# Kernel optimization log

Hardware: AMD Instinct MI355X
Metric: run time of the kernel (lower is better)

Reference implementation:

```python
import jax, jax.numpy as jnp
import numpy as np

DEPTH, DIM, M_DIM, K = 3, 16, 16, 8  # depth, emb_dim, EGNN m_dim default, num_nearest_neighbors
LN_EPS = 1e-5


def _gather(x, idx):
    # x: [B,L,...], idx: [B,L,K] -> [B,L,K,...] (per-batch neighbor gather)
    return jax.vmap(lambda xb, ib: xb[ib])(x, idx)


def _lin(k, fi, fo):
    k1, k2 = jax.random.split(k)
    lim = 1.0 / np.sqrt(fi)
    w = jax.random.uniform(k1, (fi, fo), minval=-lim, maxval=lim, dtype=jnp.float32)
    b = jax.random.uniform(k2, (fo,), minval=-lim, maxval=lim, dtype=jnp.float32)
    return w, b


def _stacked(k, fi, fo):
    ws, bs = zip(*[_lin(kk, fi, fo) for kk in jax.random.split(k, DEPTH)])
    return jnp.stack(ws), jnp.stack(bs)


def setup_inputs() -> dict:
    key = jax.random.key(0)
    ks = jax.random.split(key, 16)
    B, L, num_tokens = 16, 1024, 2
    edge_in = 2 * DIM + 1  # feats_i, feats_j, rel_dist
    inp = {}
    inp['coords'] = jax.random.normal(ks[0], (B, L, 3), dtype=jnp.float32) * 3.0
    inp['residues'] = jax.random.randint(ks[1], (B, L), 0, num_tokens)
    inp['lengths'] = jax.random.randint(ks[2], (B,), L // 2, L + 1)
    inp['token_emb'] = jax.random.normal(ks[3], (num_tokens, DIM), dtype=jnp.float32)
    inp['pos_emb'] = jax.random.normal(ks[4], (L, DIM), dtype=jnp.float32)
    inp['edge_w1'], inp['edge_b1'] = _stacked(ks[5], edge_in, edge_in * 2)
    inp['edge_w2'], inp['edge_b2'] = _stacked(ks[6], edge_in * 2, M_DIM)
    inp['coors_w1'], inp['coors_b1'] = _stacked(ks[7], M_DIM, M_DIM * 4)
    inp['coors_w2'], inp['coors_b2'] = _stacked(ks[8], M_DIM * 4, 1)
    inp['ln_g'] = jnp.ones((DEPTH, DIM), jnp.float32)
    inp['ln_b'] = jnp.zeros((DEPTH, DIM), jnp.float32)
    inp['node_w1'], inp['node_b1'] = _stacked(ks[9], DIM + M_DIM, DIM * 2)
    inp['node_w2'], inp['node_b2'] = _stacked(ks[10], DIM * 2, DIM)
    inp['final_w'], inp['final_b'] = _lin(ks[11], DIM, 3)
    return inp


def reference(coords, residues, lengths, token_emb, pos_emb,
              edge_w1, edge_b1, edge_w2, edge_b2,
              coors_w1, coors_b1, coors_w2, coors_b2,
              ln_g, ln_b, node_w1, node_b1, node_w2, node_b2,
              final_w, final_b):
    B, L, _ = coords.shape
    silu = jax.nn.silu
    mask = jnp.arange(L)[None, :] < lengths[:, None]                 # [B,L]
    pair_mask = mask[:, :, None] & mask[:, None, :]                  # [B,L,L]
    eye = jnp.eye(L, dtype=bool)
    # chain adjacency: i <-> i+1 where both endpoints are within length
    r = jnp.arange(L - 1)
    chain = jnp.zeros((L, L), bool).at[r, r + 1].set(True)
    chain = chain | chain.T
    adj = (chain[None] & pair_mask) & ~eye                           # [B,L,L]

    feats = token_emb[residues] + pos_emb[None, :L]                  # [B,L,D]
    coors = coords
    for d in range(DEPTH):
        # pairwise squared distances for kNN ranking (memory-bound)
        rel_dist_full = jnp.sum((coors[:, :, None] - coors[:, None, :]) ** 2, -1)  # [B,L,L]
        ranking = jnp.where(pair_mask, rel_dist_full, 1e5)
        ranking = jnp.where(eye, -1.0, ranking)   # self always selected first
        ranking = jnp.where(adj, 0.0, ranking)    # adjacency edges forced in
        _, idx = jax.lax.top_k(-ranking, K)                           # [B,L,K] smallest
        mask_j = _gather(mask, idx)
        emask = mask[:, :, None] & mask_j                             # [B,L,K] (valid_radius=inf)
        coors_j = _gather(coors, idx)                                 # [B,L,K,3]
        rel_coors = coors[:, :, None] - coors_j                       # [B,L,K,3]
        rel_dist = jnp.sum(rel_coors ** 2, -1, keepdims=True)         # [B,L,K,1]
        feats_j = _gather(feats, idx)                                 # [B,L,K,D]
        feats_i = jnp.broadcast_to(feats[:, :, None], feats_j.shape)
        edge_in = jnp.concatenate([feats_i, feats_j, rel_dist], -1)   # [B,L,K,2D+1]
        h = silu(edge_in @ edge_w1[d] + edge_b1[d])
        m_ij = silu(h @ edge_w2[d] + edge_b2[d])                      # [B,L,K,M]
        # equivariant coordinate update
        w = silu(m_ij @ coors_w1[d] + coors_b1[d]) @ coors_w2[d] + coors_b2[d]
        w = jnp.where(emask[..., None], w, 0.0)[..., 0]               # [B,L,K]
        coors = coors + jnp.einsum('blk,blkc->blc', w, rel_coors)
        # node update (norm_feats=True in EGNN_Network -> LayerNorm)
        m_i = jnp.sum(jnp.where(emask[..., None], m_ij, 0.0), 2)      # [B,L,M]
        mu = feats.mean(-1, keepdims=True)
        var = jnp.mean((feats - mu) ** 2, -1, keepdims=True)
        normed = (feats - mu) / jnp.sqrt(var + LN_EPS) * ln_g[d] + ln_b[d]
        nin = jnp.concatenate([normed, m_i], -1)                      # [B,L,D+M]
        feats = feats + (silu(nin @ node_w1[d] + node_b1[d]) @ node_w2[d] + node_b2[d])
    delta = feats @ final_w + final_b                                 # [B,L,3]
    return delta
```

## Files before the change

kernel.cpp:

```cpp
#include <hip/hip_runtime.h>
#include <math.h>

typedef unsigned long long u64;
typedef unsigned int u32;

#define NB 16
#define SL 1024
#define DIM 16
#define MDIM 16
#define KNN 8
#define CH 64
#define NHID 32
#define LN_EPS 1e-5f
#define PST 144

__device__ __forceinline__ float silu_f(float x) {
    const float e = __expf(-x);
    return x * __builtin_amdgcn_rcpf(1.0f + e);
}

__global__ __launch_bounds__(256) void init_kernel(
    const float* __restrict__ coords, const int* __restrict__ residues,
    const float* __restrict__ token_emb, const float* __restrict__ pos_emb,
    const float* __restrict__ w1tp, const float* __restrict__ g_eb1,
    float* __restrict__ coordsA, float* __restrict__ featsA,
    float* __restrict__ Pout)
{
    const int t = blockIdx.x * 256 + threadIdx.x;
    const int node = t >> 2;
    const int part = t & 3;
    const int l = node & (SL - 1);
    const int r = residues[node];
    float f[16];
    {
        const float4* te = (const float4*)(token_emb + (size_t)r * DIM);
        const float4* pe = (const float4*)(pos_emb + (size_t)l * DIM);
#pragma unroll
        for (int q = 0; q < 4; ++q) {
            float4 a = te[q], b4 = pe[q];
            f[4*q+0] = a.x + b4.x; f[4*q+1] = a.y + b4.y;
            f[4*q+2] = a.z + b4.z; f[4*q+3] = a.w + b4.w;
        }
    }
    if (part == 0) {
        float4* fo = (float4*)(featsA + (size_t)node * DIM);
#pragma unroll
        for (int q = 0; q < 4; ++q)
            fo[q] = make_float4(f[4*q], f[4*q+1], f[4*q+2], f[4*q+3]);
        coordsA[node * 3 + 0] = coords[node * 3 + 0];
        coordsA[node * 3 + 1] = coords[node * 3 + 1];
        coordsA[node * 3 + 2] = coords[node * 3 + 2];
    }
    const int ubase = (part & 1) * 33;
    const int wbase = (part < 2) ? 0 : 66;
    float res[36];
    res[33] = 0.f; res[34] = 0.f; res[35] = 0.f;
#pragma unroll
    for (int oo = 0; oo < 33; ++oo) {
        const int u = ubase + oo;
        const float* wr = w1tp + (wbase + u) * 16;
        float a0 = (part < 2) ? g_eb1[u] : 0.0f;
        float a1 = 0.f, a2 = 0.f, a3 = 0.f;
#pragma unroll
        for (int c = 0; c < 16; c += 4) {
            a0 = fmaf(f[c + 0], wr[c + 0], a0);
            a1 = fmaf(f[c + 1], wr[c + 1], a1);
            a2 = fmaf(f[c + 2], wr[c + 2], a2);
            a3 = fmaf(f[c + 3], wr[c + 3], a3);
        }
        res[oo] = (a0 + a1) + (a2 + a3);
    }
    float4* op = (float4*)(Pout + (size_t)node * PST + part * 36);
#pragma unroll
    for (int q = 0; q < 9; ++q)
        op[q] = make_float4(res[4*q], res[4*q+1], res[4*q+2], res[4*q+3]);
}

__global__ __launch_bounds__(256) void pack_kernel(
    const float* __restrict__ ew1, const float* __restrict__ ew2,
    const float* __restrict__ cw1,
    const float* __restrict__ nw1, const float* __restrict__ nw2,
    float* __restrict__ w1tp, float* __restrict__ w1rp, float* __restrict__ w2p,
    float* __restrict__ cw1t, float* __restrict__ nw1t, float* __restrict__ nw2t)
{
    const int stride = gridDim.x * 256;
    const int t0 = blockIdx.x * 256 + threadIdx.x;
    for (int idx = t0; idx < 3 * 132 * 16; idx += stride) {
        int d = idx / (132 * 16); int r = idx - d * 132 * 16; int o = r >> 4; int c = r & 15;
        int u = (o < 66) ? o : (o - 66);
        int cc = (o < 66) ? c : (16 + c);
        w1tp[idx] = ew1[(d * 33 + cc) * 66 + u];
    }
    for (int idx = t0; idx < 3 * 72; idx += stride) {
        int d = idx / 72; int o = idx - d * 72; int hh = o / 36; int uu = o - hh * 36;
        w1rp[idx] = (uu < 33) ? ew1[(d * 33 + 32) * 66 + hh * 33 + uu] : 0.0f;
    }
    for (int idx = t0; idx < 3 * 72 * 16; idx += stride) {
        int d = idx / (72 * 16); int r = idx - d * 72 * 16; int u = r >> 4; int v = r & 15;
        int hh = u / 36; int uu = u - hh * 36;
        w2p[idx] = (uu < 33) ? ew2[(d * 66 + hh * 33 + uu) * 16 + v] : 0.0f;
    }
    for (int idx = t0; idx < 3 * CH * 16; idx += stride) {
        int d = idx / (CH * 16); int r = idx - d * CH * 16; int t = r >> 4; int v = r & 15;
        cw1t[(d * CH + t) * 16 + v] = cw1[(d * 16 + v) * CH + t];
    }
    for (int idx = t0; idx < 3 * NHID * 32; idx += stride) {
        int d = idx / (NHID * 32); int r = idx - d * NHID * 32; int u = r >> 5; int c = r & 31;
        nw1t[(d * NHID + u) * 32 + c] = nw1[(d * 32 + c) * NHID + u];
    }
    for (int idx = t0; idx < 3 * 16 * 32; idx += stride) {
        int d = idx / (16 * 32); int r = idx - d * 16 * 32; int c = r >> 5; int u = r & 31;
        nw2t[(d * 16 + c) * 32 + u] = nw2[(d * 32 + u) * 16 + c];
    }
}

__device__ __forceinline__ void merge8(u32* a, const u32* bb) {
    u32 c[8];
#pragma unroll
    for (int t = 0; t < 8; ++t) c[t] = min(a[t], bb[7 - t]);
#define MCAS(x, y) { u32 mn = min(c[x], c[y]); u32 mx = max(c[x], c[y]); c[x] = mn; c[y] = mx; }
    MCAS(0, 4) MCAS(1, 5) MCAS(2, 6) MCAS(3, 7)
    MCAS(0, 2) MCAS(1, 3) MCAS(4, 6) MCAS(5, 7)
    MCAS(0, 1) MCAS(2, 3) MCAS(4, 5) MCAS(6, 7)
#undef MCAS
#pragma unroll
    for (int t = 0; t < 8; ++t) a[t] = c[t];
}

__global__ __launch_bounds__(1024) void knn_kernel(
    const float* __restrict__ coords, const int* __restrict__ lengths,
    int* __restrict__ idxbuf)
{
    __shared__ __align__(16) float4 s_cand[SL];
    __shared__ u32 lists[16][64][9];
    const int tid = threadIdx.x;
    const int b = blockIdx.x >> 4;
    const int i0 = (blockIdx.x & 15) << 6;
    const int len = lengths[b];
    const float* cb = coords + (size_t)b * SL * 3;
    for (int idx = tid; idx < SL; idx += 1024) {
        const float* cp = cb + idx * 3;
        s_cand[idx] = make_float4(cp[0], cp[1], cp[2], 0.0f);
    }
    __syncthreads();

    const int wv = tid >> 6;
    const int lane = tid & 63;
    const int i = i0 + lane;
    const bool mi = i < len;
    const float4 qi = s_cand[i];
    const float xi = qi.x, yi = qi.y, zi = qi.z;

    u32 lst[8];
#pragma unroll
    for (int t = 0; t < 8; ++t) lst[t] = 0xFFFFFFFFu;

    const int jbase = wv << 6;
#pragma unroll 4
    for (int jj = 0; jj < 64; ++jj) {
        const int j = jbase + jj;
        const float4 cj = s_cand[j];
        const float dx = xi - cj.x, dy = yi - cj.y, dz = zi - cj.z;
        const float dist = dx * dx + dy * dy + dz * dz;
        const int dij = j - i;
        const bool pm = mi && (j < len);
        const bool adjx = (dij == 1) | (dij == -1);
        float v = pm ? (adjx ? 0.0f : dist) : 1e5f;
        v = (dij == 0) ? -1.0f : v;
        u32 bits = __float_as_uint(v);
        bits ^= (u32)((int)bits >> 31) | 0x80000000u;
        const u32 key = (bits & 0xFFFFFC00u) | (u32)j;
#pragma unroll
        for (int p = 7; p >= 1; --p)
            lst[p] = min(max(key, lst[p - 1]), lst[p]);
        lst[0] = min(key, lst[0]);
    }

#pragma unroll
    for (int t = 0; t < 8; ++t) lists[wv][lane][t] = lst[t];
    __syncthreads();

    if (tid < 512) {
        const int p = tid >> 6, q = tid & 63;
        u32 a[8], bb[8];
#pragma unroll
        for (int t = 0; t < 8; ++t) { a[t] = lists[2 * p][q][t]; bb[t] = lists[2 * p + 1][q][t]; }
        merge8(a, bb);
#pragma unroll
        for (int t = 0; t < 8; ++t) lists[2 * p][q][t] = a[t];
    }
    __syncthreads();
    if (tid < 256) {
        const int p = tid >> 6, q = tid & 63;
        u32 a[8], bb[8];
#pragma unroll
        for (int t = 0; t < 8; ++t) { a[t] = lists[4 * p][q][t]; bb[t] = lists[4 * p + 2][q][t]; }
        merge8(a, bb);
#pragma unroll
        for (int t = 0; t < 8; ++t) lists[4 * p][q][t] = a[t];
    }
    __syncthreads();
    if (tid < 128) {
        const int p = tid >> 6, q = tid & 63;
        u32 a[8], bb[8];
#pragma unroll
        for (int t = 0; t < 8; ++t) { a[t] = lists[8 * p][q][t]; bb[t] = lists[8 * p + 4][q][t]; }
        merge8(a, bb);
#pragma unroll
        for (int t = 0; t < 8; ++t) lists[8 * p][q][t] = a[t];
    }
    __syncthreads();
    if (tid < 64) {
        const int q = tid;
        u32 a[8], bb[8];
#pragma unroll
        for (int t = 0; t < 8; ++t) { a[t] = lists[0][q][t]; bb[t] = lists[8][q][t]; }
        merge8(a, bb);
        const size_t node = (size_t)b * SL + i0 + q;
        int4 r0 = make_int4((int)(a[0] & 1023u), (int)(a[1] & 1023u), (int)(a[2] & 1023u), (int)(a[3] & 1023u));
        int4 r1 = make_int4((int)(a[4] & 1023u), (int)(a[5] & 1023u), (int)(a[6] & 1023u), (int)(a[7] & 1023u));
        ((int4*)idxbuf)[node * 2 + 0] = r0;
        ((int4*)idxbuf)[node * 2 + 1] = r1;
    }
}

__global__ __launch_bounds__(256, 4) void layer_kernel(
    const int d,
    const float* __restrict__ coordsIn, float* __restrict__ coordsOut,
    const float* __restrict__ featsIn, float* __restrict__ featsOut,
    const float* __restrict__ Pbuf,
    const int* __restrict__ idxbuf, const int* __restrict__ lengths,
    const float* __restrict__ w1rp, const float* __restrict__ w2p,
    const float* __restrict__ g_eb2,
    const float* __restrict__ cw1t, const float* __restrict__ g_cb1,
    const float* __restrict__ g_cw2, const float* __restrict__ g_cb2,
    const float* __restrict__ g_lng, const float* __restrict__ g_lnb,
    const float* __restrict__ nw1t, const float* __restrict__ g_nb1,
    const float* __restrict__ nw2t, const float* __restrict__ g_nb2,
    const float* __restrict__ w1tp_all, const float* __restrict__ g_eb1,
    float* __restrict__ PbufOut)
{
    __shared__ float s_w2e[72 * 16];
    __shared__ float s_w1r[72];
    __shared__ float s_cw1[CH * 16];
    __shared__ float s_cw2v[CH];
    __shared__ float s_nw1[NHID * 36];
    __shared__ float s_nw2[16 * 36];
    __shared__ float s_eb2[16], s_cb1[CH];
    __shared__ float s_lng[16], s_lnb[16], s_nb1[32], s_nb2[16];
    __shared__ float s_cb2v;

    const int tid = threadIdx.x;
    for (int t = tid; t < 72 * 16; t += 256) s_w2e[t] = w2p[d * 72 * 16 + t];
    for (int t = tid; t < CH * 16; t += 256) s_cw1[t] = cw1t[d * CH * 16 + t];
    for (int t = tid; t < NHID * 32; t += 256) s_nw1[(t >> 5) * 36 + (t & 31)] = nw1t[d * NHID * 32 + t];
    for (int t = tid; t < 16 * 32; t += 256) s_nw2[(t >> 5) * 36 + (t & 31)] = nw2t[d * 16 * 32 + t];
    if (tid < 72) s_w1r[tid] = w1rp[d * 72 + tid];
    if (tid < CH) { s_cw2v[tid] = g_cw2[d * CH + tid]; s_cb1[tid] = g_cb1[d * CH + tid]; }
    if (tid < 16) {
        s_eb2[tid] = g_eb2[d * 16 + tid];
        s_lng[tid] = g_lng[d * 16 + tid];
        s_lnb[tid] = g_lnb[d * 16 + tid];
        s_nb2[tid] = g_nb2[d * 16 + tid];
    }
    if (tid < 32) s_nb1[tid] = g_nb1[d * 32 + tid];
    if (tid == 0) s_cb2v = g_cb2[d];

    const int lane = tid & 63;
    const int h = (lane >> 3) & 1;
    const int k = lane & 7;
    const int n = blockIdx.x * 16 + (tid >> 4);
    const int b = n >> 10;
    const int i = n & (SL - 1);
    const int len = lengths[b];
    const int j = idxbuf[n * 8 + k];
    const bool em = (i < len) && (j < len);

    float fi[16];
    {
        const float4* pp = (const float4*)(featsIn + (size_t)n * DIM);
        float4 a = pp[0], c2 = pp[1], c3 = pp[2], c4 = pp[3];
        fi[0]=a.x; fi[1]=a.y; fi[2]=a.z; fi[3]=a.w;
        fi[4]=c2.x; fi[5]=c2.y; fi[6]=c2.z; fi[7]=c2.w;
        fi[8]=c3.x; fi[9]=c3.y; fi[10]=c3.z; fi[11]=c3.w;
        fi[12]=c4.x; fi[13]=c4.y; fi[14]=c4.z; fi[15]=c4.w;
    }
    float ci[3], rel[3];
    {
        const float* cp = coordsIn + (size_t)n * 3;
        const float* cq = coordsIn + ((size_t)b * SL + j) * 3;
        ci[0] = cp[0]; ci[1] = cp[1]; ci[2] = cp[2];
        rel[0] = ci[0] - cq[0]; rel[1] = ci[1] - cq[1]; rel[2] = ci[2] - cq[2];
    }
    const float rd = fmaf(rel[0], rel[0], fmaf(rel[1], rel[1], rel[2] * rel[2]));

    const int ub = h * 36;
    const float* PiP = Pbuf + (size_t)n * PST + ub;
    const float* PjP = Pbuf + ((size_t)b * SL + j) * PST + 72 + ub;
    float4 pa = *(const float4*)PiP;
    float4 pb = *(const float4*)PjP;

    __syncthreads();

    float macc[16];
#pragma unroll
    for (int v = 0; v < 16; ++v) macc[v] = h ? 0.0f : s_eb2[v];
#pragma unroll
    for (int c4 = 0; c4 < 9; ++c4) {
        float4 na, nb;
        if (c4 < 8) {
            na = *(const float4*)(PiP + 4 * (c4 + 1));
            nb = *(const float4*)(PjP + 4 * (c4 + 1));
        }
        const int u0 = ub + c4 * 4;
        const float hu0 = silu_f(fmaf(rd, s_w1r[u0 + 0], pa.x + pb.x));
        const float hu1 = silu_f(fmaf(rd, s_w1r[u0 + 1], pa.y + pb.y));
        const float hu2 = silu_f(fmaf(rd, s_w1r[u0 + 2], pa.z + pb.z));
        const float hu3 = silu_f(fmaf(rd, s_w1r[u0 + 3], pa.w + pb.w));
        const float* w2r = &s_w2e[u0 * 16];
#pragma unroll
        for (int v = 0; v < 16; ++v) {
            float m0 = fmaf(hu0, w2r[v], macc[v]);
            float m1 = fmaf(hu1, w2r[16 + v], m0);
            float m2 = fmaf(hu2, w2r[32 + v], m1);
            macc[v] = fmaf(hu3, w2r[48 + v], m2);
        }
        if (c4 < 8) { pa = na; pb = nb; }
    }

    float mm[16];
#pragma unroll
    for (int v = 0; v < 16; ++v)
        mm[v] = silu_f(macc[v] + __shfl_xor(macc[v], 8, 64));

    const int tb = h * 32;
    float wa = 0.f;
#pragma unroll 4
    for (int tt = 0; tt < 32; ++tt) {
        const float* cr = &s_cw1[(tb + tt) * 16];
        float a0 = s_cb1[tb + tt], a1 = 0.f;
#pragma unroll
        for (int v = 0; v < 16; v += 2) {
            a0 = fmaf(mm[v], cr[v], a0);
            a1 = fmaf(mm[v + 1], cr[v + 1], a1);
        }
        wa = fmaf(silu_f(a0 + a1), s_cw2v[tb + tt], wa);
    }
    const float wao = __shfl_xor(wa, 8, 64);
    const float we = em ? (wa + wao + s_cb2v) : 0.f;

    float wr0 = we * rel[0], wr1 = we * rel[1], wr2 = we * rel[2];
#pragma unroll
    for (int s = 1; s < 8; s <<= 1) {
        wr0 += __shfl_xor(wr0, s, 64);
        wr1 += __shfl_xor(wr1, s, 64);
        wr2 += __shfl_xor(wr2, s, 64);
    }
    if ((lane & 15) == 0) {
        coordsOut[(size_t)n * 3 + 0] = ci[0] + wr0;
        coordsOut[(size_t)n * 3 + 1] = ci[1] + wr1;
        coordsOut[(size_t)n * 3 + 2] = ci[2] + wr2;
    }

    float mi_[16];
#pragma unroll
    for (int v = 0; v < 16; ++v) mi_[v] = em ? mm[v] : 0.f;
#pragma unroll
    for (int s = 1; s < 8; s <<= 1) {
#pragma unroll
        for (int v = 0; v < 16; ++v) mi_[v] += __shfl_xor(mi_[v], s, 64);
    }

    float mu = 0.f;
#pragma unroll
    for (int c = 0; c < 16; ++c) mu += fi[c];
    mu *= 0.0625f;
    float var = 0.f;
#pragma unroll
    for (int c = 0; c < 16; ++c) { const float dd = fi[c] - mu; var = fmaf(dd, dd, var); }
    var *= 0.0625f;
    const float rs = rsqrtf(var + LN_EPS);
    float nn[16];
#pragma unroll
    for (int c = 0; c < 16; ++c) nn[c] = fmaf((fi[c] - mu) * rs, s_lng[c], s_lnb[c]);

    const int sub = lane & 15;
    float nh[2];
#pragma unroll
    for (int q = 0; q < 2; ++q) {
        const int u = sub * 2 + q;
        const float* nr = &s_nw1[u * 36];
        float a0 = s_nb1[u], a1 = 0.f;
#pragma unroll
        for (int c = 0; c < 16; c += 2) {
            a0 = fmaf(nn[c], nr[c], a0);
            a1 = fmaf(nn[c + 1], nr[c + 1], a1);
        }
#pragma unroll
        for (int v = 0; v < 16; v += 2) {
            a0 = fmaf(mi_[v], nr[16 + v], a0);
            a1 = fmaf(mi_[v + 1], nr[16 + v + 1], a1);
        }
        nh[q] = silu_f(a0 + a1);
    }

    const int nbase = lane & ~15;
    const float* w2c = &s_nw2[sub * 36];
    float o0 = s_nb2[sub];
#pragma unroll
    for (int u = 0; u < 32; ++u) {
        const float v = __shfl(nh[u & 1], nbase + (u >> 1), 64);
        o0 = fmaf(v, w2c[u], o0);
    }
    const float fo = fi[sub] + o0;
    featsOut[(size_t)n * DIM + sub] = fo;

    if (d < 2) {
        float fr[16];
#pragma unroll
        for (int c = 0; c < 16; ++c) fr[c] = __shfl(fo, nbase + c, 64);
        const float* wbase = w1tp_all + (d + 1) * 132 * 16;
        const float* bbase = g_eb1 + (d + 1) * 66;
        float* Pout = PbufOut + (size_t)n * PST;
#pragma unroll
        for (int q = 0; q < 9; ++q) {
            const int col = sub + (q << 4);
            const int ch = (col >= 108) ? 3 : (col >= 72) ? 2 : (col >= 36) ? 1 : 0;
            const int uu = col - ch * 36;
            const bool valid = uu < 33;
            const int u = ((ch & 1) ? 33 : 0) + uu;
            const int uc = valid ? u : 0;
            const int widx = valid ? ((ch < 2) ? u : 66 + u) : 0;
            float a0 = (valid && ch < 2) ? bbase[uc] : 0.0f;
            float a1 = 0.f, a2 = 0.f, a3 = 0.f;
            const float* wr = wbase + widx * 16;
#pragma unroll
            for (int cc = 0; cc < 16; cc += 4) {
                a0 = fmaf(fr[cc + 0], wr[cc + 0], a0);
                a1 = fmaf(fr[cc + 1], wr[cc + 1], a1);
                a2 = fmaf(fr[cc + 2], wr[cc + 2], a2);
                a3 = fmaf(fr[cc + 3], wr[cc + 3], a3);
            }
            Pout[col] = valid ? ((a0 + a1) + (a2 + a3)) : 0.0f;
        }
    }
}

__global__ __launch_bounds__(256) void final_kernel(
    const float* __restrict__ feats, const float* __restrict__ fw,
    const float* __restrict__ fb, float* __restrict__ out)
{
    const int nid = blockIdx.x * 256 + threadIdx.x;
    if (nid >= NB * SL) return;
    float f[DIM];
#pragma unroll
    for (int c = 0; c < DIM; ++c) f[c] = feats[nid * DIM + c];
#pragma unroll
    for (int o = 0; o < 3; ++o) {
        float acc = fb[o];
#pragma unroll
        for (int c = 0; c < DIM; ++c) acc = fmaf(f[c], fw[c * 3 + o], acc);
        out[nid * 3 + o] = acc;
    }
}

extern "C" void kernel_launch(void* const* d_in, const int* in_sizes, int n_in,
                              void* d_out, int out_size, void* d_ws, size_t ws_size,
                              hipStream_t stream) {
    const float* coords    = (const float*)d_in[0];
    const int*   residues  = (const int*)d_in[1];
    const int*   lengths   = (const int*)d_in[2];
    const float* token_emb = (const float*)d_in[3];
    const float* pos_emb   = (const float*)d_in[4];
    const float* ew1 = (const float*)d_in[5];
    const float* eb1 = (const float*)d_in[6];
    const float* ew2 = (const float*)d_in[7];
    const float* eb2 = (const float*)d_in[8];
    const float* cw1 = (const float*)d_in[9];
    const float* cb1 = (const float*)d_in[10];
    const float* cw2 = (const float*)d_in[11];
    const float* cb2 = (const float*)d_in[12];
    const float* lng = (const float*)d_in[13];
    const float* lnb = (const float*)d_in[14];
    const float* nw1 = (const float*)d_in[15];
    const float* nb1 = (const float*)d_in[16];
    const float* nw2 = (const float*)d_in[17];
    const float* nb2 = (const float*)d_in[18];
    const float* fw  = (const float*)d_in[19];
    const float* fb  = (const float*)d_in[20];

    float* ws = (float*)d_ws;
    float* coordsA = ws;
    float* coordsB = coordsA + NB * SL * 3;
    float* featsA  = coordsB + NB * SL * 3;
    float* featsB  = featsA + NB * SL * DIM;
    int*   idxbuf  = (int*)(featsB + NB * SL * DIM);
    float* w1tp = (float*)(idxbuf + NB * SL * KNN);
    float* w1rp = w1tp + 3 * 132 * 16;
    float* w2p  = w1rp + 3 * 72;
    float* cw1t = w2p + 3 * 72 * 16;
    float* nw1t = cw1t + 3 * CH * 16;
    float* nw2t = nw1t + 3 * NHID * 32;
    float* PbufA = nw2t + 3 * 16 * 32;
    float* PbufB = PbufA + (size_t)NB * SL * PST;

    pack_kernel<<<32, 256, 0, stream>>>(ew1, ew2, cw1, nw1, nw2, w1tp, w1rp, w2p, cw1t, nw1t, nw2t);
    init_kernel<<<NB * SL * 4 / 256, 256, 0, stream>>>(coords, residues, token_emb, pos_emb,
                                                        w1tp, eb1, coordsA, featsA, PbufA);

    float* cIn = coordsA; float* cOut = coordsB;
    float* fIn = featsA;  float* fOut = featsB;
    float* pIn = PbufA;   float* pOut = PbufB;
    for (int d = 0; d < 3; ++d) {
        knn_kernel<<<NB * SL / 64, 1024, 0, stream>>>(cIn, lengths, idxbuf);
        layer_kernel<<<NB * SL * KNN / 128, 256, 0, stream>>>(d, cIn, cOut, fIn, fOut, pIn, idxbuf, lengths,
            w1rp, w2p, eb2, cw1t, cb1, cw2, cb2, lng, lnb, nw1t, nb1, nw2t, nb2,
            w1tp, eb1, pOut);
        float* t;
        t = cIn; cIn = cOut; cOut = t;
        t = fIn; fIn = fOut; fOut = t;
        t = pIn; pIn = pOut; pOut = t;
    }

    final_kernel<<<NB * SL / 256, 256, 0, stream>>>(fIn, fw, fb, (float*)d_out);
}
```

Before: 282.6 us.

## Fuse kNN search, layer update and final projection into one kernel per layer

Merges the separate kNN kernel into the per-layer kernel: each 256-thread block first finds neighbors for its 16 nodes (16 threads per node scanning 64-candidate chunks, then a 4-level merge tree), writes idxbuf, then reuses the same shared memory for the layer weights and runs the edge/node update. The final linear projection is folded into the last layer's epilogue, which removes the final kernel. This cuts four launches and the separate kNN pass. In exchange, each block redundantly stages all 1024 candidate coordinates for only 16 query nodes, so per-layer coordinate loading rises from 256 to 1024 block-loads, and the serial merge tree adds barriers. Shared memory use per block also grows.

Measured after the change: 248.0 us. 12.3% less time.

```diff
diff --git a/kernel.cpp b/kernel.cpp
--- a/kernel.cpp
+++ b/kernel.cpp
@@ -7,7 +7,6 @@
 #define NB 16
 #define SL 1024
 #define DIM 16
-#define MDIM 16
 #define KNN 8
 #define CH 64
 #define NHID 32
@@ -127,109 +126,12 @@
     for (int t = 0; t < 8; ++t) a[t] = c[t];
 }
 
-__global__ __launch_bounds__(1024) void knn_kernel(
-    const float* __restrict__ coords, const int* __restrict__ lengths,
-    int* __restrict__ idxbuf)
-{
-    __shared__ __align__(16) float4 s_cand[SL];
-    __shared__ u32 lists[16][64][9];
-    const int tid = threadIdx.x;
-    const int b = blockIdx.x >> 4;
-    const int i0 = (blockIdx.x & 15) << 6;
-    const int len = lengths[b];
-    const float* cb = coords + (size_t)b * SL * 3;
-    for (int idx = tid; idx < SL; idx += 1024) {
-        const float* cp = cb + idx * 3;
-        s_cand[idx] = make_float4(cp[0], cp[1], cp[2], 0.0f);
-    }
-    __syncthreads();
-
-    const int wv = tid >> 6;
-    const int lane = tid & 63;
-    const int i = i0 + lane;
-    const bool mi = i < len;
-    const float4 qi = s_cand[i];
-    const float xi = qi.x, yi = qi.y, zi = qi.z;
-
-    u32 lst[8];
-#pragma unroll
-    for (int t = 0; t < 8; ++t) lst[t] = 0xFFFFFFFFu;
-
-    const int jbase = wv << 6;
-#pragma unroll 4
-    for (int jj = 0; jj < 64; ++jj) {
-        const int j = jbase + jj;
-        const float4 cj = s_cand[j];
-        const float dx = xi - cj.x, dy = yi - cj.y, dz = zi - cj.z;
-        const float dist = dx * dx + dy * dy + dz * dz;
-        const int dij = j - i;
-        const bool pm = mi && (j < len);
-        const bool adjx = (dij == 1) | (dij == -1);
-        float v = pm ? (adjx ? 0.0f : dist) : 1e5f;
-        v = (dij == 0) ? -1.0f : v;
-        u32 bits = __float_as_uint(v);
-        bits ^= (u32)((int)bits >> 31) | 0x80000000u;
-        const u32 key = (bits & 0xFFFFFC00u) | (u32)j;
-#pragma unroll
-        for (int p = 7; p >= 1; --p)
-            lst[p] = min(max(key, lst[p - 1]), lst[p]);
-        lst[0] = min(key, lst[0]);
-    }
-
-#pragma unroll
-    for (int t = 0; t < 8; ++t) lists[wv][lane][t] = lst[t];
-    __syncthreads();
-
-    if (tid < 512) {
-        const int p = tid >> 6, q = tid & 63;
-        u32 a[8], bb[8];
-#pragma unroll
-        for (int t = 0; t < 8; ++t) { a[t] = lists[2 * p][q][t]; bb[t] = lists[2 * p + 1][q][t]; }
-        merge8(a, bb);
-#pragma unroll
-        for (int t = 0; t < 8; ++t) lists[2 * p][q][t] = a[t];
-    }
-    __syncthreads();
-    if (tid < 256) {
-        const int p = tid >> 6, q = tid & 63;
-        u32 a[8], bb[8];
-#pragma unroll
-        for (int t = 0; t < 8; ++t) { a[t] = lists[4 * p][q][t]; bb[t] = lists[4 * p + 2][q][t]; }
-        merge8(a, bb);
-#pragma unroll
-        for (int t = 0; t < 8; ++t) lists[4 * p][q][t] = a[t];
-    }
-    __syncthreads();
-    if (tid < 128) {
-        const int p = tid >> 6, q = tid & 63;
-        u32 a[8], bb[8];
-#pragma unroll
-        for (int t = 0; t < 8; ++t) { a[t] = lists[8 * p][q][t]; bb[t] = lists[8 * p + 4][q][t]; }
-        merge8(a, bb);
-#pragma unroll
-        for (int t = 0; t < 8; ++t) lists[8 * p][q][t] = a[t];
-    }
-    __syncthreads();
-    if (tid < 64) {
-        const int q = tid;
-        u32 a[8], bb[8];
-#pragma unroll
-        for (int t = 0; t < 8; ++t) { a[t] = lists[0][q][t]; bb[t] = lists[8][q][t]; }
-        merge8(a, bb);
-        const size_t node = (size_t)b * SL + i0 + q;
-        int4 r0 = make_int4((int)(a[0] & 1023u), (int)(a[1] & 1023u), (int)(a[2] & 1023u), (int)(a[3] & 1023u));
-        int4 r1 = make_int4((int)(a[4] & 1023u), (int)(a[5] & 1023u), (int)(a[6] & 1023u), (int)(a[7] & 1023u));
-        ((int4*)idxbuf)[node * 2 + 0] = r0;
-        ((int4*)idxbuf)[node * 2 + 1] = r1;
-    }
-}
-
-__global__ __launch_bounds__(256, 4) void layer_kernel(
+__global__ __launch_bounds__(256, 4) void fused_kernel(
     const int d,
     const float* __restrict__ coordsIn, float* __restrict__ coordsOut,
     const float* __restrict__ featsIn, float* __restrict__ featsOut,
-    const float* __restrict__ Pbuf,
-    const int* __restrict__ idxbuf, const int* __restrict__ lengths,
+    const float* __restrict__ Pbuf, float* __restrict__ PbufOut,
+    int* __restrict__ idxbuf, const int* __restrict__ lengths,
     const float* __restrict__ w1rp, const float* __restrict__ w2p,
     const float* __restrict__ g_eb2,
     const float* __restrict__ cw1t, const float* __restrict__ g_cb1,
@@ -238,229 +140,335 @@
     const float* __restrict__ nw1t, const float* __restrict__ g_nb1,
     const float* __restrict__ nw2t, const float* __restrict__ g_nb2,
     const float* __restrict__ w1tp_all, const float* __restrict__ g_eb1,
-    float* __restrict__ PbufOut)
+    const float* __restrict__ fw, const float* __restrict__ fb,
+    float* __restrict__ gout)
 {
-    __shared__ float s_w2e[72 * 16];
-    __shared__ float s_w1r[72];
-    __shared__ float s_cw1[CH * 16];
-    __shared__ float s_cw2v[CH];
-    __shared__ float s_nw1[NHID * 36];
-    __shared__ float s_nw2[16 * 36];
-    __shared__ float s_eb2[16], s_cb1[CH];
-    __shared__ float s_lng[16], s_lnb[16], s_nb1[32], s_nb2[16];
-    __shared__ float s_cb2v;
-
+    __shared__ __align__(16) char smem[25600];
     const int tid = threadIdx.x;
-    for (int t = tid; t < 72 * 16; t += 256) s_w2e[t] = w2p[d * 72 * 16 + t];
-    for (int t = tid; t < CH * 16; t += 256) s_cw1[t] = cw1t[d * CH * 16 + t];
-    for (int t = tid; t < NHID * 32; t += 256) s_nw1[(t >> 5) * 36 + (t & 31)] = nw1t[d * NHID * 32 + t];
-    for (int t = tid; t < 16 * 32; t += 256) s_nw2[(t >> 5) * 36 + (t & 31)] = nw2t[d * 16 * 32 + t];
-    if (tid < 72) s_w1r[tid] = w1rp[d * 72 + tid];
-    if (tid < CH) { s_cw2v[tid] = g_cw2[d * CH + tid]; s_cb1[tid] = g_cb1[d * CH + tid]; }
-    if (tid < 16) {
-        s_eb2[tid] = g_eb2[d * 16 + tid];
-        s_lng[tid] = g_lng[d * 16 + tid];
-        s_lnb[tid] = g_lnb[d * 16 + tid];
-        s_nb2[tid] = g_nb2[d * 16 + tid];
-    }
-    if (tid < 32) s_nb1[tid] = g_nb1[d * 32 + tid];
-    if (tid == 0) s_cb2v = g_cb2[d];
-
     const int lane = tid & 63;
-    const int h = (lane >> 3) & 1;
-    const int k = lane & 7;
-    const int n = blockIdx.x * 16 + (tid >> 4);
-    const int b = n >> 10;
-    const int i = n & (SL - 1);
-    const int len = lengths[b];
-    const int j = idxbuf[n * 8 + k];
-    const bool em = (i < len) && (j < len);
-
-    float fi[16];
+
     {
-        const float4* pp = (const float4*)(featsIn + (size_t)n * DIM);
-        float4 a = pp[0], c2 = pp[1], c3 = pp[2], c4 = pp[3];
-        fi[0]=a.x; fi[1]=a.y; fi[2]=a.z; fi[3]=a.w;
-        fi[4]=c2.x; fi[5]=c2.y; fi[6]=c2.z; fi[7]=c2.w;
-        fi[8]=c3.x; fi[9]=c3.y; fi[10]=c3.z; fi[11]=c3.w;
-        fi[12]=c4.x; fi[13]=c4.y; fi[14]=c4.z; fi[15]=c4.w;
-    }
-    float ci[3], rel[3];
+        float4* s_cand = (float4*)smem;
+        u32* lst_base  = (u32*)(smem + 16384);
+        const int bk = blockIdx.x >> 6;
+        const int i0 = (blockIdx.x & 63) << 4;
+        const int len = lengths[bk];
+        const float* cb = coordsIn + (size_t)bk * SL * 3;
+        for (int idx = tid; idx < SL; idx += 256) {
+            const float* cp = cb + idx * 3;
+            s_cand[idx] = make_float4(cp[0], cp[1], cp[2], 0.0f);
+        }
+        __syncthreads();
+
+        const int q = tid & 15;
+        const int s = tid >> 4;
+        const int i = i0 + q;
+        const bool mi = i < len;
+        const float4 qi = s_cand[i];
+        const float xi = qi.x, yi = qi.y, zi = qi.z;
+
+        u32 lst[8];
+#pragma unroll
+        for (int t = 0; t < 8; ++t) lst[t] = 0xFFFFFFFFu;
+
+        const int jbase = s << 6;
+#pragma unroll 4
+        for (int jj = 0; jj < 64; ++jj) {
+            const int j = jbase + jj;
+            const float4 cj = s_cand[j];
+            const float dx = xi - cj.x, dy = yi - cj.y, dz = zi - cj.z;
+            const float dist = dx * dx + dy * dy + dz * dz;
+            const int dij = j - i;
+            const bool pm = mi && (j < len);
+            const bool adjx = (dij == 1) | (dij == -1);
+            float v = pm ? (adjx ? 0.0f : dist) : 1e5f;
+            v = (dij == 0) ? -1.0f : v;
+            u32 bits = __float_as_uint(v);
+            bits ^= (u32)((int)bits >> 31) | 0x80000000u;
+            const u32 key = (bits & 0xFFFFFC00u) | (u32)j;
+#pragma unroll
+            for (int p = 7; p >= 1; --p)
+                lst[p] = min(max(key, lst[p - 1]), lst[p]);
+            lst[0] = min(key, lst[0]);
+        }
+#pragma unroll
+        for (int t = 0; t < 8; ++t) lst_base[(s * 16 + q) * 9 + t] = lst[t];
+        __syncthreads();
+
+        if (tid < 128) {
+            const int p = tid >> 4, qq = tid & 15;
+            u32 a[8], bb[8];
+#pragma unroll
+            for (int t = 0; t < 8; ++t) {
+                a[t]  = lst_base[((2 * p) * 16 + qq) * 9 + t];
+                bb[t] = lst_base[((2 * p + 1) * 16 + qq) * 9 + t];
+            }
+            merge8(a, bb);
+#pragma unroll
+            for (int t = 0; t < 8; ++t) lst_base[((2 * p) * 16 + qq) * 9 + t] = a[t];
+        }
+        __syncthreads();
+        if (tid < 64) {
+            const int p = tid >> 4, qq = tid & 15;
+            u32 a[8], bb[8];
+#pragma unroll
+            for (int t = 0; t < 8; ++t) {
+                a[t]  = lst_base[((4 * p) * 16 + qq) * 9 + t];
+                bb[t] = lst_base[((4 * p + 2) * 16 + qq) * 9 + t];
+            }
+            merge8(a, bb);
+#pragma unroll
+            for (int t = 0; t < 8; ++t) lst_base[((4 * p) * 16 + qq) * 9 + t] = a[t];
+        }
+        __syncthreads();
+        if (tid < 32) {
+            const int p = tid >> 4, qq = tid & 15;
+            u32 a[8], bb[8];
+#pragma unroll
+            for (int t = 0; t < 8; ++t) {
+                a[t]  = lst_base[((8 * p) * 16 + qq) * 9 + t];
+                bb[t] = lst_base[((8 * p + 4) * 16 + qq) * 9 + t];
+            }
+            merge8(a, bb);
+#pragma unroll
+            for (int t = 0; t < 8; ++t) lst_base[((8 * p) * 16 + qq) * 9 + t] = a[t];
+        }
+        __syncthreads();
+        if (tid < 16) {
+            const int qq = tid;
+            u32 a[8], bb[8];
+#pragma unroll
+            for (int t = 0; t < 8; ++t) {
+                a[t]  = lst_base[(0 * 16 + qq) * 9 + t];
+                bb[t] = lst_base[(8 * 16 + qq) * 9 + t];
+            }
+            merge8(a, bb);
+            const size_t node = (size_t)bk * SL + i0 + qq;
+            int4 r0 = make_int4((int)(a[0] & 1023u), (int)(a[1] & 1023u), (int)(a[2] & 1023u), (int)(a[3] & 1023u));
+            int4 r1 = make_int4((int)(a[4] & 1023u), (int)(a[5] & 1023u), (int)(a[6] & 1023u), (int)(a[7] & 1023u));
+            ((int4*)idxbuf)[node * 2 + 0] = r0;
+            ((int4*)idxbuf)[node * 2 + 1] = r1;
+        }
+    }
+    __syncthreads();
+
     {
-        const float* cp = coordsIn + (size_t)n * 3;
-        const float* cq = coordsIn + ((size_t)b * SL + j) * 3;
-        ci[0] = cp[0]; ci[1] = cp[1]; ci[2] = cp[2];
-        rel[0] = ci[0] - cq[0]; rel[1] = ci[1] - cq[1]; rel[2] = ci[2] - cq[2];
-    }
-    const float rd = fmaf(rel[0], rel[0], fmaf(rel[1], rel[1], rel[2] * rel[2]));
-
-    const int ub = h * 36;
-    const float* PiP = Pbuf + (size_t)n * PST + ub;
-    const float* PjP = Pbuf + ((size_t)b * SL + j) * PST + 72 + ub;
-    float4 pa = *(const float4*)PiP;
-    float4 pb = *(const float4*)PjP;
-
-    __syncthreads();
-
-    float macc[16];
-#pragma unroll
-    for (int v = 0; v < 16; ++v) macc[v] = h ? 0.0f : s_eb2[v];
-#pragma unroll
-    for (int c4 = 0; c4 < 9; ++c4) {
-        float4 na, nb;
-        if (c4 < 8) {
-            na = *(const float4*)(PiP + 4 * (c4 + 1));
-            nb = *(const float4*)(PjP + 4 * (c4 + 1));
-        }
-        const int u0 = ub + c4 * 4;
-        const float hu0 = silu_f(fmaf(rd, s_w1r[u0 + 0], pa.x + pb.x));
-        const float hu1 = silu_f(fmaf(rd, s_w1r[u0 + 1], pa.y + pb.y));
-        const float hu2 = silu_f(fmaf(rd, s_w1r[u0 + 2], pa.z + pb.z));
-        const float hu3 = silu_f(fmaf(rd, s_w1r[u0 + 3], pa.w + pb.w));
-        const float* w2r = &s_w2e[u0 * 16];
+        float* s_w2e  = (float*)(smem);
+        float* s_cw1  = (float*)(smem + 4608);
+        float* s_nw1  = (float*)(smem + 8704);
+        float* s_nw2  = (float*)(smem + 13312);
+        float* s_w1r  = (float*)(smem + 15616);
+        float* s_cw2v = (float*)(smem + 15904);
+        float* s_cb1  = (float*)(smem + 16160);
+        float* s_eb2  = (float*)(smem + 16416);
+        float* s_lng  = (float*)(smem + 16480);
+        float* s_lnb  = (float*)(smem + 16544);
+        float* s_nb1  = (float*)(smem + 16608);
+        float* s_nb2  = (float*)(smem + 16736);
+        float* s_cb2  = (float*)(smem + 16800);
+
+        for (int t = tid; t < 72 * 16; t += 256) s_w2e[t] = w2p[d * 72 * 16 + t];
+        for (int t = tid; t < CH * 16; t += 256) s_cw1[t] = cw1t[d * CH * 16 + t];
+        for (int t = tid; t < NHID * 32; t += 256) s_nw1[(t >> 5) * 36 + (t & 31)] = nw1t[d * NHID * 32 + t];
+        for (int t = tid; t < 16 * 32; t += 256) s_nw2[(t >> 5) * 36 + (t & 31)] = nw2t[d * 16 * 32 + t];
+        if (tid < 72) s_w1r[tid] = w1rp[d * 72 + tid];
+        if (tid < CH) { s_cw2v[tid] = g_cw2[d * CH + tid]; s_cb1[tid] = g_cb1[d * CH + tid]; }
+        if (tid < 16) {
+            s_eb2[tid] = g_eb2[d * 16 + tid];
+            s_lng[tid] = g_lng[d * 16 + tid];
+            s_lnb[tid] = g_lnb[d * 16 + tid];
+            s_nb2[tid] = g_nb2[d * 16 + tid];
+        }
+        if (tid < 32) s_nb1[tid] = g_nb1[d * 32 + tid];
+        if (tid == 0) s_cb2[0] = g_cb2[d];
+
+        const int h = (lane >> 3) & 1;
+        const int k = lane & 7;
+        const int sub = lane & 15;
+        const int n = blockIdx.x * 16 + (tid >> 4);
+        const int b = n >> 10;
+        const int len = lengths[b];
+        const int j = idxbuf[n * 8 + k];
+        const bool em = ((n & 1023) < len) && (j < len);
+
+        float ci[3], rel[3];
+        {
+            const float* cp = coordsIn + (size_t)n * 3;
+            const float* cq = coordsIn + ((size_t)b * SL + j) * 3;
+            ci[0] = cp[0]; ci[1] = cp[1]; ci[2] = cp[2];
+            rel[0] = ci[0] - cq[0]; rel[1] = ci[1] - cq[1]; rel[2] = ci[2] - cq[2];
+        }
+        const float rd = fmaf(rel[0], rel[0], fmaf(rel[1], rel[1], rel[2] * rel[2]));
+
+        const int ub = h * 36;
+        const float* PiP = Pbuf + (size_t)n * PST + ub;
+        const float* PjP = Pbuf + ((size_t)b * SL + j) * PST + 72 + ub;
+        float4 pa = *(const float4*)PiP;
+        float4 pb = *(const float4*)PjP;
+
+        __syncthreads();
+
+        float macc[16];
+#pragma unroll
+        for (int v = 0; v < 16; ++v) macc[v] = h ? 0.0f : s_eb2[v];
+#pragma unroll
+        for (int c4 = 0; c4 < 9; ++c4) {
+            float4 na, nb;
+            if (c4 < 8) {
+                na = *(const float4*)(PiP + 4 * (c4 + 1));
+                nb = *(const float4*)(PjP + 4 * (c4 + 1));
+            }
+            const int u0 = ub + c4 * 4;
+            const float4 w1r4 = *(const float4*)&s_w1r[u0];
+            const float hu0 = silu_f(fmaf(rd, w1r4.x, pa.x + pb.x));
+            const float hu1 = silu_f(fmaf(rd, w1r4.y, pa.y + pb.y));
+            const float hu2 = silu_f(fmaf(rd, w1r4.z, pa.z + pb.z));
+            const float hu3 = silu_f(fmaf(rd, w1r4.w, pa.w + pb.w));
+            const float* w2r = &s_w2e[u0 * 16];
+#pragma unroll
+            for (int v = 0; v < 16; ++v) {
+                float m0 = fmaf(hu0, w2r[v], macc[v]);
+                float m1 = fmaf(hu1, w2r[16 + v], m0);
+                float m2 = fmaf(hu2, w2r[32 + v], m1);
+                macc[v] = fmaf(hu3, w2r[48 + v], m2);
+            }
+            if (c4 < 8) { pa = na; pb = nb; }
+        }
+
+#pragma unroll
+        for (int v = 0; v < 16; ++v)
+            macc[v] = silu_f(macc[v] + __shfl_xor(macc[v], 8, 64));
+
+        const int tb = h * 32;
+        float wa = 0.f;
+#pragma unroll 4
+        for (int tt = 0; tt < 32; ++tt) {
+            const float* cr = &s_cw1[(tb + tt) * 16];
+            float a0 = s_cb1[tb + tt], a1 = 0.f;
+#pragma unroll
+            for (int v = 0; v < 16; v += 2) {
+                a0 = fmaf(macc[v], cr[v], a0);
+                a1 = fmaf(macc[v + 1], cr[v + 1], a1);
+            }
+            wa = fmaf(silu_f(a0 + a1), s_cw2v[tb + tt], wa);
+        }
+        const float wao = __shfl_xor(wa, 8, 64);
+        const float we = em ? (wa + wao + s_cb2[0]) : 0.f;
+
+        float wr0 = we * rel[0], wr1 = we * rel[1], wr2 = we * rel[2];
+#pragma unroll
+        for (int s = 1; s < 8; s <<= 1) {
+            wr0 += __shfl_xor(wr0, s, 64);
+            wr1 += __shfl_xor(wr1, s, 64);
+            wr2 += __shfl_xor(wr2, s, 64);
+        }
+        if ((lane & 15) == 0) {
+            coordsOut[(size_t)n * 3 + 0] = ci[0] + wr0;
+            coordsOut[(size_t)n * 3 + 1] = ci[1] + wr1;
+            coordsOut[(size_t)n * 3 + 2] = ci[2] + wr2;
+        }
+
 #pragma unroll
         for (int v = 0; v < 16; ++v) {
-            float m0 = fmaf(hu0, w2r[v], macc[v]);
-            float m1 = fmaf(hu1, w2r[16 + v], m0);
-            float m2 = fmaf(hu2, w2r[32 + v], m1);
-            macc[v] = fmaf(hu3, w2r[48 + v], m2);
-        }
-        if (c4 < 8) { pa = na; pb = nb; }
-    }
-
-    float mm[16];
-#pragma unroll
-    for (int v = 0; v < 16; ++v)
-        mm[v] = silu_f(macc[v] + __shfl_xor(macc[v], 8, 64));
-
-    const int tb = h * 32;
-    float wa = 0.f;
-#pragma unroll 4
-    for (int tt = 0; tt < 32; ++tt) {
-        const float* cr = &s_cw1[(tb + tt) * 16];
-        float a0 = s_cb1[tb + tt], a1 = 0.f;
-#pragma unroll
-        for (int v = 0; v < 16; v += 2) {
-            a0 = fmaf(mm[v], cr[v], a0);
-            a1 = fmaf(mm[v + 1], cr[v + 1], a1);
-        }
-        wa = fmaf(silu_f(a0 + a1), s_cw2v[tb + tt], wa);
-    }
-    const float wao = __shfl_xor(wa, 8, 64);
-    const float we = em ? (wa + wao + s_cb2v) : 0.f;
-
-    float wr0 = we * rel[0], wr1 = we * rel[1], wr2 = we * rel[2];
-#pragma unroll
-    for (int s = 1; s < 8; s <<= 1) {
-        wr0 += __shfl_xor(wr0, s, 64);
-        wr1 += __shfl_xor(wr1, s, 64);
-        wr2 += __shfl_xor(wr2, s, 64);
-    }
-    if ((lane & 15) == 0) {
-        coordsOut[(size_t)n * 3 + 0] = ci[0] + wr0;
-        coordsOut[(size_t)n * 3 + 1] = ci[1] + wr1;
-        coordsOut[(size_t)n * 3 + 2] = ci[2] + wr2;
-    }
-
-    float mi_[16];
-#pragma unroll
-    for (int v = 0; v < 16; ++v) mi_[v] = em ? mm[v] : 0.f;
-#pragma unroll
-    for (int s = 1; s < 8; s <<= 1) {
-#pragma unroll
-        for (int v = 0; v < 16; ++v) mi_[v] += __shfl_xor(mi_[v], s, 64);
-    }
-
-    float mu = 0.f;
-#pragma unroll
-    for (int c = 0; c < 16; ++c) mu += fi[c];
-    mu *= 0.0625f;
-    float var = 0.f;
-#pragma unroll
-    for (int c = 0; c < 16; ++c) { const float dd = fi[c] - mu; var = fmaf(dd, dd, var); }
-    var *= 0.0625f;
-    const float rs = rsqrtf(var + LN_EPS);
-    float nn[16];
-#pragma unroll
-    for (int c = 0; c < 16; ++c) nn[c] = fmaf((fi[c] - mu) * rs, s_lng[c], s_lnb[c]);
-
-    const int sub = lane & 15;
-    float nh[2];
-#pragma unroll
-    for (int q = 0; q < 2; ++q) {
-        const int u = sub * 2 + q;
-        const float* nr = &s_nw1[u * 36];
-        float a0 = s_nb1[u], a1 = 0.f;
-#pragma unroll
-        for (int c = 0; c < 16; c += 2) {
-            a0 = fmaf(nn[c], nr[c], a0);
-            a1 = fmaf(nn[c + 1], nr[c + 1], a1);
-        }
-#pragma unroll
-        for (int v = 0; v < 16; v += 2) {
-            a0 = fmaf(mi_[v], nr[16 + v], a0);
-            a1 = fmaf(mi_[v + 1], nr[16 + v + 1], a1);
-        }
-        nh[q] = silu_f(a0 + a1);
-    }
-
-    const int nbase = lane & ~15;
-    const float* w2c = &s_nw2[sub * 36];
-    float o0 = s_nb2[sub];
-#pragma unroll
-    for (int u = 0; u < 32; ++u) {
-        const float v = __shfl(nh[u & 1], nbase + (u >> 1), 64);
-        o0 = fmaf(v, w2c[u], o0);
-    }
-    const float fo = fi[sub] + o0;
-    featsOut[(size_t)n * DIM + sub] = fo;
-
-    if (d < 2) {
+            macc[v] = em ? macc[v] : 0.f;
+#pragma unroll
+            for (int s = 1; s < 8; s <<= 1)
+                macc[v] += __shfl_xor(macc[v], s, 64);
+        }
+
+        float fi[16];
+        {
+            const float4* pp = (const float4*)(featsIn + (size_t)n * DIM);
+            float4 a0 = pp[0], a1 = pp[1], a2 = pp[2], a3 = pp[3];
+            fi[0]=a0.x; fi[1]=a0.y; fi[2]=a0.z; fi[3]=a0.w;
+            fi[4]=a1.x; fi[5]=a1.y; fi[6]=a1.z; fi[7]=a1.w;
+            fi[8]=a2.x; fi[9]=a2.y; fi[10]=a2.z; fi[11]=a2.w;
+            fi[12]=a3.x; fi[13]=a3.y; fi[14]=a3.z; fi[15]=a3.w;
+        }
+        const float fiSub = featsIn[(size_t)n * DIM + sub];
+
+        {
+            float mu = 0.f;
+#pragma unroll
+            for (int c = 0; c < 16; ++c) mu += fi[c];
+            mu *= 0.0625f;
+            float var = 0.f;
+#pragma unroll
+            for (int c = 0; c < 16; ++c) { const float dd = fi[c] - mu; var = fmaf(dd, dd, var); }
+            var *= 0.0625f;
+            const float rs = rsqrtf(var + LN_EPS);
+#pragma unroll
+            for (int c = 0; c < 16; ++c) fi[c] = fmaf((fi[c] - mu) * rs, s_lng[c], s_lnb[c]);
+        }
+
+        float nh[2];
+#pragma unroll
+        for (int q2 = 0; q2 < 2; ++q2) {
+            const int u = sub * 2 + q2;
+            const float* nr = &s_nw1[u * 36];
+            float a0 = s_nb1[u], a1 = 0.f;
+#pragma unroll
+            for (int c = 0; c < 16; c += 2) {
+                a0 = fmaf(fi[c], nr[c], a0);
+                a1 = fmaf(fi[c + 1], nr[c + 1], a1);
+            }
+#pragma unroll
+            for (int v = 0; v < 16; v += 2) {
+                a0 = fmaf(macc[v], nr[16 + v], a0);
+                a1 = fmaf(macc[v + 1], nr[16 + v + 1], a1);
+            }
+            nh[q2] = silu_f(a0 + a1);
+        }
+
+        const int nbase = lane & ~15;
+        const float* w2c = &s_nw2[sub * 36];
+        float o0 = s_nb2[sub];
+#pragma unroll
+        for (int u = 0; u < 32; ++u) {
+            const float v = __shfl(nh[u & 1], nbase + (u >> 1), 64);
+            o0 = fmaf(v, w2c[u], o0);
+        }
+        const float fo = fiSub + o0;
+        featsOut[(size_t)n * DIM + sub] = fo;
+
         float fr[16];
 #pragma unroll
         for (int c = 0; c < 16; ++c) fr[c] = __shfl(fo, nbase + c, 64);
-        const float* wbase = w1tp_all + (d + 1) * 132 * 16;
-        const float* bbase = g_eb1 + (d + 1) * 66;
-        float* Pout = PbufOut + (size_t)n * PST;
-#pragma unroll
-        for (int q = 0; q < 9; ++q) {
-            const int col = sub + (q << 4);
-            const int ch = (col >= 108) ? 3 : (col >= 72) ? 2 : (col >= 36) ? 1 : 0;
-            const int uu = col - ch * 36;
-            const bool valid = uu < 33;
-            const int u = ((ch & 1) ? 33 : 0) + uu;
-            const int uc = valid ? u : 0;
-            const int widx = valid ? ((ch < 2) ? u : 66 + u) : 0;
-            float a0 = (valid && ch < 2) ? bbase[uc] : 0.0f;
-            float a1 = 0.f, a2 = 0.f, a3 = 0.f;
-            const float* wr = wbase + widx * 16;
-#pragma unroll
-            for (int cc = 0; cc < 16; cc += 4) {
-                a0 = fmaf(fr[cc + 0], wr[cc + 0], a0);
-                a1 = fmaf(fr[cc + 1], wr[cc + 1], a1);
-                a2 = fmaf(fr[cc + 2], wr[cc + 2], a2);
-                a3 = fmaf(fr[cc + 3], wr[cc + 3], a3);
-            }
-            Pout[col] = valid ? ((a0 + a1) + (a2 + a3)) : 0.0f;
-        }
-    }
-}
-
-__global__ __launch_bounds__(256) void final_kernel(
-    const float* __restrict__ feats, const float* __restrict__ fw,
-    const float* __restrict__ fb, float* __restrict__ out)
-{
-    const int nid = blockIdx.x * 256 + threadIdx.x;
-    if (nid >= NB * SL) return;
-    float f[DIM];
-#pragma unroll
-    for (int c = 0; c < DIM; ++c) f[c] = feats[nid * DIM + c];
-#pragma unroll
-    for (int o = 0; o < 3; ++o) {
-        float acc = fb[o];
-#pragma unroll
-        for (int c = 0; c < DIM; ++c) acc = fmaf(f[c], fw[c * 3 + o], acc);
-        out[nid * 3 + o] = acc;
+
+        if (d < 2) {
+            const float* wbase = w1tp_all + (d + 1) * 132 * 16;
+            const float* bbase = g_eb1 + (d + 1) * 66;
+            float* Pout = PbufOut + (size_t)n * PST;
+#pragma unroll
+            for (int q2 = 0; q2 < 9; ++q2) {
+                const int col = sub + (q2 << 4);
+                const int ch = (col >= 108) ? 3 : (col >= 72) ? 2 : (col >= 36) ? 1 : 0;
+                const int uu = col - ch * 36;
+                const bool valid = uu < 33;
+                const int u = ((ch & 1) ? 33 : 0) + uu;
+                const int uc = valid ? u : 0;
+                const int widx = valid ? ((ch < 2) ? u : 66 + u) : 0;
+                float a0 = (valid && ch < 2) ? bbase[uc] : 0.0f;
+                float a1 = 0.f, a2 = 0.f, a3 = 0.f;
+                const float* wr = wbase + widx * 16;
+#pragma unroll
+                for (int cc = 0; cc < 16; cc += 4) {
+                    a0 = fmaf(fr[cc + 0], wr[cc + 0], a0);
+                    a1 = fmaf(fr[cc + 1], wr[cc + 1], a1);
+                    a2 = fmaf(fr[cc + 2], wr[cc + 2], a2);
+                    a3 = fmaf(fr[cc + 3], wr[cc + 3], a3);
+                }
+                Pout[col] = valid ? ((a0 + a1) + (a2 + a3)) : 0.0f;
+            }
+        } else {
+            if (sub < 3) {
+                float acc = fb[sub];
+#pragma unroll
+                for (int c = 0; c < 16; ++c)
+                    acc = fmaf(fr[c], fw[c * 3 + sub], acc);
+                gout[(size_t)n * 3 + sub] = acc;
+            }
+        }
     }
 }
 
@@ -503,6 +511,7 @@
     float* nw2t = nw1t + 3 * NHID * 32;
     float* PbufA = nw2t + 3 * 16 * 32;
     float* PbufB = PbufA + (size_t)NB * SL * PST;
+    float* gout  = (float*)d_out;
 
     pack_kernel<<<32, 256, 0, stream>>>(ew1, ew2, cw1, nw1, nw2, w1tp, w1rp, w2p, cw1t, nw1t, nw2t);
     init_kernel<<<NB * SL * 4 / 256, 256, 0, stream>>>(coords, residues, token_emb, pos_emb,
@@ -512,15 +521,13 @@
     float* fIn = featsA;  float* fOut = featsB;
     float* pIn = PbufA;   float* pOut = PbufB;
     for (int d = 0; d < 3; ++d) {
-        knn_kernel<<<NB * SL / 64, 1024, 0, stream>>>(cIn, lengths, idxbuf);
-        layer_kernel<<<NB * SL * KNN / 128, 256, 0, stream>>>(d, cIn, cOut, fIn, fOut, pIn, idxbuf, lengths,
+        fused_kernel<<<NB * SL / 16, 256, 0, stream>>>(d, cIn, cOut, fIn, fOut, pIn, pOut,
+            idxbuf, lengths,
             w1rp, w2p, eb2, cw1t, cb1, cw2, cb2, lng, lnb, nw1t, nb1, nw2t, nb2,
-            w1tp, eb1, pOut);
+            w1tp, eb1, fw, fb, gout);
         float* t;
         t = cIn; cIn = cOut; cOut = t;
         t = fIn; fIn = fOut; fOut = t;
         t = pIn; pIn = pOut; pOut = t;
     }
-
-    final_kernel<<<NB * SL / 256, 256, 0, stream>>>(fIn, fw, fb, (float*)d_out);
 }
```
